# Performance work log

Measured on AMD Instinct MI355X. Metric: run time of the kernel, lower is better.

The kernel has to match this reference:

```python
import jax, jax.numpy as jnp
import numpy as np

T, H, I, E, TOPK = 8192, 2048, 4096, 8, 2

def setup_inputs() -> dict:
    key = jax.random.key(0)
    k1, k2, k3, k4 = jax.random.split(key, 4)
    x = jax.random.normal(k1, (T, H), dtype=jnp.float32)
    gate_w = jax.random.normal(k2, (E, H), dtype=jnp.float32) * 0.02
    ws = jax.random.normal(k3, (E, 2 * I, H), dtype=jnp.float32) * 0.02
    w2s = jax.random.normal(k4, (E, H, I), dtype=jnp.float32) * 0.02
    return {"x": x, "gate_w": gate_w, "ws": ws, "w2s": w2s, "top_k": TOPK}

def reference(x, gate_w, ws, w2s, top_k):
    num_tokens = x.shape[0]
    num_experts = ws.shape[0]
    inter = w2s.shape[2]
    # --- router (fused_topk): softmax -> top-k -> renormalize ---
    logits = x @ gate_w.T                       # [T, E]
    probs = jax.nn.softmax(logits, axis=-1)
    topk_w, topk_ids = jax.lax.top_k(probs, top_k)   # [T, K]
    if top_k > 1:
        topk_w = topk_w / jnp.sum(topk_w, axis=-1, keepdims=True)
    # dense combine-weights [E, T]: sum of routing weights per (token, expert)
    tok = jnp.arange(num_tokens)
    cw = jnp.zeros((num_tokens, num_experts), dtype=x.dtype)
    cw = cw.at[tok[:, None], topk_ids].add(topk_w)
    cw = cw.T                                   # [E, T]
    # --- fused_experts: per-expert gated-SiLU MLP, weighted combine ---
    def body(acc, inp):
        e_ws, e_w2, e_cw = inp                  # [2I,H], [H,I], [T]
        gu = x @ e_ws.T                         # [T, 2I]
        g, u = gu[:, :inter], gu[:, inter:]
        h = jax.nn.silu(g) * u                  # SiluAndMul
        out = h @ e_w2.T                        # [T, H]
        return acc + e_cw[:, None] * out, None
    init = jnp.zeros_like(x)
    final, _ = jax.lax.scan(body, init, (ws, w2s, cw))
    return final
```

## Files before the change

kernel.cpp:

```cpp
#include <hip/hip_runtime.h>
#include <hip/hip_fp16.h>
#include <cstdint>
#include <cstddef>

#define TTOK 8192
#define HD   2048
#define ID   4096
#define NE   8
#define NPAIR (TTOK * 2)
#define PADROWS 18432

typedef _Float16 h8 __attribute__((ext_vector_type(8)));
typedef float    f4 __attribute__((ext_vector_type(4)));

#define VMWAIT(n) asm volatile("s_waitcnt vmcnt(" #n ")" ::: "memory")
#define MEMFENCE  asm volatile("" ::: "memory")
#define BAR()     __builtin_amdgcn_s_barrier()

__device__ __forceinline__ void async_cp16(const void* g, void* l) {
  __builtin_amdgcn_global_load_lds(
      (const __attribute__((address_space(1))) unsigned int*)g,
      (__attribute__((address_space(3))) unsigned int*)l, 16, 0, 0);
}

__device__ __forceinline__ f4 zero4() { f4 z = {0.f, 0.f, 0.f, 0.f}; return z; }

template <bool NT>
__global__ void cvt_kernel(const float* __restrict__ src, _Float16* __restrict__ dst, size_t n) {
  size_t stride = (size_t)gridDim.x * blockDim.x * 8;
  for (size_t i = ((size_t)blockIdx.x * blockDim.x + threadIdx.x) * 8; i < n; i += stride) {
    const float4* s = (const float4*)(src + i);
    float4 a = s[0], b = s[1];
    h8 o;
    o[0] = (_Float16)a.x; o[1] = (_Float16)a.y; o[2] = (_Float16)a.z; o[3] = (_Float16)a.w;
    o[4] = (_Float16)b.x; o[5] = (_Float16)b.y; o[6] = (_Float16)b.z; o[7] = (_Float16)b.w;
    if constexpr (NT) __builtin_nontemporal_store(o, (h8*)(dst + i));
    else *(h8*)(dst + i) = o;
  }
}

__global__ __launch_bounds__(256) void gate_kernel(
    const float* __restrict__ x, const float* __restrict__ gw,
    int* __restrict__ counts, int* __restrict__ tids, float* __restrict__ tw) {
  int lane = threadIdx.x & 63;
  int t = blockIdx.x * 4 + (threadIdx.x >> 6);
  const float* xr = x + (size_t)t * HD;
  float acc[NE];
#pragma unroll
  for (int e = 0; e < NE; e++) acc[e] = 0.f;
  for (int j = lane; j < HD; j += 64) {
    float xv = xr[j];
#pragma unroll
    for (int e = 0; e < NE; e++) acc[e] += xv * gw[e * HD + j];
  }
#pragma unroll
  for (int off = 32; off > 0; off >>= 1) {
#pragma unroll
    for (int e = 0; e < NE; e++) acc[e] += __shfl_xor(acc[e], off, 64);
  }
  if (lane == 0) {
    int e0 = 0; float v0 = acc[0];
#pragma unroll
    for (int e = 1; e < NE; e++) if (acc[e] > v0) { v0 = acc[e]; e0 = e; }
    int e1 = -1; float v1 = -1e30f;
#pragma unroll
    for (int e = 0; e < NE; e++) if (e != e0 && acc[e] > v1) { v1 = acc[e]; e1 = e; }
    float b = __expf(v1 - v0);
    float w0 = 1.f / (1.f + b);
    tids[2 * t] = e0; tids[2 * t + 1] = e1;
    tw[2 * t] = w0;   tw[2 * t + 1] = b * w0;
    atomicAdd(&counts[e0], 1); atomicAdd(&counts[e1], 1);
  }
}

__global__ void scan_kernel(const int* __restrict__ counts, int* __restrict__ offs,
                            int* __restrict__ cursor) {
  if (threadIdx.x == 0 && blockIdx.x == 0) {
    int off = 0;
    for (int e = 0; e < NE; e++) {
      offs[e] = off; cursor[e] = off;
      off += ((counts[e] + 255) >> 8) << 8;
    }
    offs[NE] = off;
  }
}

__global__ void scatter_kernel(const int* __restrict__ tids, const float* __restrict__ tw,
                               int* __restrict__ cursor, int* __restrict__ perm,
                               float* __restrict__ pw, int* __restrict__ pairpos) {
  int t = blockIdx.x * 256 + threadIdx.x;
#pragma unroll
  for (int k = 0; k < 2; k++) {
    int e = tids[2 * t + k];
    int pos = atomicAdd(&cursor[e], 1);
    perm[pos] = t; pw[pos] = tw[2 * t + k];
    pairpos[2 * t + k] = pos;
  }
}

__global__ void padfill_kernel(const int* __restrict__ counts, const int* __restrict__ offs,
                               int* __restrict__ perm) {
  int s = blockIdx.x * 256 + threadIdx.x;
#pragma unroll
  for (int e = 0; e < NE; e++) {
    if (s >= offs[e] + counts[e] && s < offs[e + 1]) perm[s] = -1;
  }
}

#define LA(BB, H) ((BB) * 65536 + (H) * 16384)
#define LB(BB, H) ((BB) * 65536 + 32768 + (H) * 16384)
#define RD(boff) (*(const h8*)(smem + (boff)))

#define LOAD_AF(BB, MH) do { \
  af[0][0] = RD(LA(BB,MH) + amoff + 0*2048 + sa0); \
  af[0][1] = RD(LA(BB,MH) + amoff + 0*2048 + sa1); \
  af[1][0] = RD(LA(BB,MH) + amoff + 1*2048 + sa0); \
  af[1][1] = RD(LA(BB,MH) + amoff + 1*2048 + sa1); \
  af[2][0] = RD(LA(BB,MH) + amoff + 2*2048 + sa0); \
  af[2][1] = RD(LA(BB,MH) + amoff + 2*2048 + sa1); \
  af[3][0] = RD(LA(BB,MH) + amoff + 3*2048 + sa0); \
  af[3][1] = RD(LA(BB,MH) + amoff + 3*2048 + sa1); } while (0)

#define LOAD_BF(BB, NH) do { \
  bf[0][0] = RD(LB(BB,NH) + bnoff + 0*2048 + sa0); \
  bf[0][1] = RD(LB(BB,NH) + bnoff + 0*2048 + sa1); \
  bf[1][0] = RD(LB(BB,NH) + bnoff + 1*2048 + sa0); \
  bf[1][1] = RD(LB(BB,NH) + bnoff + 1*2048 + sa1); } while (0)

#define MM(MH,NH,M,N) \
  acc[MH][NH][M][N] = __builtin_amdgcn_mfma_f32_16x16x32_f16(af[M][0], bf[N][0], acc[MH][NH][M][N], 0, 0, 0); \
  acc[MH][NH][M][N] = __builtin_amdgcn_mfma_f32_16x16x32_f16(af[M][1], bf[N][1], acc[MH][NH][M][N], 0, 0, 0);

#define MFMAQ(MH,NH) do { __builtin_amdgcn_s_setprio(1); \
  MM(MH,NH,0,0) MM(MH,NH,0,1) MM(MH,NH,1,0) MM(MH,NH,1,1) \
  MM(MH,NH,2,0) MM(MH,NH,2,1) MM(MH,NH,3,0) MM(MH,NH,3,1) \
  __builtin_amdgcn_s_setprio(0); } while (0)

#define STG(gp, ldsbyte, kt) do { \
  async_cp16(gp[0] + (size_t)(kt) * 64, smem + (ldsbyte) + (wid * 2 + 0) * 1024 + lane * 16); \
  async_cp16(gp[1] + (size_t)(kt) * 64, smem + (ldsbyte) + (wid * 2 + 1) * 1024 + lane * 16); } while (0)

#define ACC_ZERO() do { \
  _Pragma("unroll") for (int mh = 0; mh < 2; mh++) \
  _Pragma("unroll") for (int nh = 0; nh < 2; nh++) \
  _Pragma("unroll") for (int m = 0; m < 4; m++) \
  _Pragma("unroll") for (int n = 0; n < 2; n++) acc[mh][nh][m][n] = zero4(); } while (0)

#define KLOOP(NI) \
  STG(gA[0], LA(0,0), 0); STG(gA[1], LA(0,1), 0); \
  STG(gB[0], LB(0,0), 0); STG(gB[1], LB(0,1), 0); \
  STG(gA[0], LA(1,0), 1); STG(gB[1], LB(1,1), 1); \
  VMWAIT(4); \
  BAR(); \
  for (int i = 0; i < (NI); ++i) { \
    bool last = (i == (NI) - 1); \
    int kt1 = 2 * i + 1, kt2 = 2 * i + 2, kt3 = 2 * i + 3; \
     \
    MEMFENCE; LOAD_AF(0,0); LOAD_BF(0,0); \
    STG(gA[1], LA(1,1), kt1); STG(gB[0], LB(1,0), kt1); \
    BAR(); MEMFENCE; MFMAQ(0,0); BAR(); \
     \
    MEMFENCE; LOAD_BF(0,1); \
    BAR(); MEMFENCE; MFMAQ(0,1); BAR(); \
     \
    MEMFENCE; LOAD_AF(0,1); \
    if (!last) STG(gA[0], LA(0,0), kt2); \
    BAR(); MEMFENCE; MFMAQ(1,1); BAR(); \
     \
    MEMFENCE; LOAD_BF(0,0); \
    if (!last) { STG(gB[1], LB(0,1), kt2); VMWAIT(4); } else { VMWAIT(0); } \
    BAR(); MEMFENCE; MFMAQ(1,0); BAR(); \
     \
    MEMFENCE; LOAD_AF(1,0); LOAD_BF(1,0); \
    if (!last) { STG(gA[1], LA(0,1), kt2); STG(gB[0], LB(0,0), kt2); } \
    BAR(); MEMFENCE; MFMAQ(0,0); BAR(); \
     \
    MEMFENCE; LOAD_BF(1,1); \
    BAR(); MEMFENCE; MFMAQ(0,1); BAR(); \
     \
    MEMFENCE; LOAD_AF(1,1); \
    if (!last) STG(gA[0], LA(1,0), kt3); \
    BAR(); MEMFENCE; MFMAQ(1,1); BAR(); \
     \
    MEMFENCE; LOAD_BF(1,0); \
    if (!last) { STG(gB[1], LB(1,1), kt3); VMWAIT(4); } \
    BAR(); MEMFENCE; MFMAQ(1,0); BAR(); \
  }

__global__ __launch_bounds__(512, 2) void gemm1_kernel(
    const _Float16* __restrict__ xh, const _Float16* __restrict__ wsh,
    const int* __restrict__ counts, const int* __restrict__ offs,
    const int* __restrict__ perm, _Float16* __restrict__ hb) {
  int bx = blockIdx.x, by = blockIdx.y;
  int e = by >> 5, rb = by & 31;
  if (rb >= ((counts[e] + 255) >> 8)) return;
  int row0 = offs[e] + (rb << 8);
  int n0 = bx << 7;

  __shared__ char smem[131072];
  int tid = threadIdx.x, lane = tid & 63, wid = tid >> 6;
  int wm = wid >> 2, wn = wid & 3;
  int lr = lane & 15, ks = lane >> 4;
  int sa0 = lr * 128 + (((ks)     ^ (lr & 7)) << 4);
  int sa1 = lr * 128 + (((ks + 4) ^ (lr & 7)) << 4);
  int amoff = wm * 8192;
  int bnoff = wn * 4096;

  int srow = wid * 16 + (lane >> 3);
  int scol = ((lane & 7) ^ (lane >> 3)) * 8;
  const _Float16* gA[2][2]; const _Float16* gB[2][2];
#pragma unroll
  for (int h = 0; h < 2; h++)
#pragma unroll
    for (int j = 0; j < 2; j++) {
      int r = row0 + h * 128 + srow + j * 8;
      int pv = perm[r]; if (pv < 0) pv = 0;
      gA[h][j] = xh + (size_t)pv * HD + scol;
      gB[h][j] = wsh + ((size_t)e * 2 * ID + (size_t)h * ID + n0 + srow + j * 8) * HD + scol;
    }

  f4 acc[2][2][4][2];
  h8 af[4][2], bf[2][2];
  ACC_ZERO();

  KLOOP(16)

#pragma unroll
  for (int mh = 0; mh < 2; mh++)
#pragma unroll
    for (int m = 0; m < 4; m++)
#pragma unroll
      for (int n = 0; n < 2; n++)
#pragma unroll
        for (int r = 0; r < 4; r++) {
          float g = acc[mh][0][m][n][r], u = acc[mh][1][m][n][r];
          float hv = g / (1.f + __expf(-g)) * u;
          int row = row0 + mh * 128 + wm * 64 + m * 16 + ks * 4 + r;
          int col = n0 + wn * 32 + n * 16 + lr;
          __builtin_nontemporal_store((_Float16)hv, hb + (size_t)row * ID + col);
        }
}

__global__ __launch_bounds__(512, 2) void gemm2_kernel(
    const _Float16* __restrict__ hb, const _Float16* __restrict__ w2h,
    const int* __restrict__ counts, const int* __restrict__ offs,
    _Float16* __restrict__ hb2) {
  int bx = blockIdx.x, by = blockIdx.y;
  int e = by >> 5, rb = by & 31;
  if (rb >= ((counts[e] + 255) >> 8)) return;
  int row0 = offs[e] + (rb << 8);
  int n0 = bx << 8;

  __shared__ char smem[131072];
  int tid = threadIdx.x, lane = tid & 63, wid = tid >> 6;
  int wm = wid >> 2, wn = wid & 3;
  int lr = lane & 15, ks = lane >> 4;
  int sa0 = lr * 128 + (((ks)     ^ (lr & 7)) << 4);
  int sa1 = lr * 128 + (((ks + 4) ^ (lr & 7)) << 4);
  int amoff = wm * 8192;
  int bnoff = wn * 4096;

  int srow = wid * 16 + (lane >> 3);
  int scol = ((lane & 7) ^ (lane >> 3)) * 8;
  const _Float16* gA[2][2]; const _Float16* gB[2][2];
#pragma unroll
  for (int h = 0; h < 2; h++)
#pragma unroll
    for (int j = 0; j < 2; j++) {
      gA[h][j] = hb + ((size_t)(row0 + h * 128 + srow + j * 8)) * ID + scol;
      gB[h][j] = w2h + ((size_t)e * HD + n0 + h * 128 + srow + j * 8) * ID + scol;
    }

  f4 acc[2][2][4][2];
  h8 af[4][2], bf[2][2];
  ACC_ZERO();

  KLOOP(32)

#pragma unroll
  for (int mh = 0; mh < 2; mh++)
#pragma unroll
    for (int nh = 0; nh < 2; nh++)
#pragma unroll
      for (int m = 0; m < 4; m++)
#pragma unroll
        for (int n = 0; n < 2; n++)
#pragma unroll
          for (int r = 0; r < 4; r++) {
            int row = row0 + mh * 128 + wm * 64 + m * 16 + ks * 4 + r;
            int col = n0 + nh * 128 + wn * 32 + n * 16 + lr;
            __builtin_nontemporal_store((_Float16)acc[mh][nh][m][n][r],
                                        hb2 + (size_t)row * HD + col);
          }
}

__global__ __launch_bounds__(256) void combine_kernel(
    const _Float16* __restrict__ hb2, const int* __restrict__ pairpos,
    const float* __restrict__ pw, float* __restrict__ out) {
  int i = blockIdx.x * 256 + threadIdx.x;
  int t = i >> 8, g = (i & 255) * 8;
  int p0 = pairpos[2 * t], p1 = pairpos[2 * t + 1];
  float w0 = pw[p0], w1 = pw[p1];
  h8 a = *(const h8*)(hb2 + (size_t)p0 * HD + g);
  h8 b = *(const h8*)(hb2 + (size_t)p1 * HD + g);
  f4 o0, o1;
  o0[0] = w0 * (float)a[0] + w1 * (float)b[0];
  o0[1] = w0 * (float)a[1] + w1 * (float)b[1];
  o0[2] = w0 * (float)a[2] + w1 * (float)b[2];
  o0[3] = w0 * (float)a[3] + w1 * (float)b[3];
  o1[0] = w0 * (float)a[4] + w1 * (float)b[4];
  o1[1] = w0 * (float)a[5] + w1 * (float)b[5];
  o1[2] = w0 * (float)a[6] + w1 * (float)b[6];
  o1[3] = w0 * (float)a[7] + w1 * (float)b[7];
  __builtin_nontemporal_store(o0, (f4*)(out + (size_t)t * HD + g));
  __builtin_nontemporal_store(o1, (f4*)(out + (size_t)t * HD + g + 4));
}

extern "C" void kernel_launch(void* const* d_in, const int* in_sizes, int n_in,
                              void* d_out, int out_size, void* d_ws, size_t ws_size,
                              hipStream_t stream) {
  const float* x   = (const float*)d_in[0];
  const float* gw  = (const float*)d_in[1];
  const float* wsf = (const float*)d_in[2];
  const float* w2f = (const float*)d_in[3];

  int* counts   = (int*)d_ws;
  int* offs     = counts + 8;
  int* cursor   = offs + 16;
  int* tids     = cursor + 8;
  float* tw     = (float*)(tids + NPAIR);
  int* perm     = (int*)(tw + NPAIR);
  float* pw     = (float*)(perm + PADROWS);
  int* pairpos  = (int*)(pw + PADROWS);

  char* base = (char*)d_ws;
  size_t off_xh  = (size_t)512 * 1024;
  size_t off_hb  = off_xh + (size_t)TTOK * HD * 2;
  size_t off_big = off_hb + (size_t)PADROWS * ID * 2;
  size_t need    = off_big + (size_t)NE * 2 * ID * HD * 2;
  if (ws_size < need) return;

  _Float16* xh  = (_Float16*)(base + off_xh);
  _Float16* hb  = (_Float16*)(base + off_hb);
  _Float16* wsh = (_Float16*)(base + off_big);
  _Float16* w2h = (_Float16*)(base + off_big);
  _Float16* hb2 = (_Float16*)(base + off_big + (size_t)NE * HD * ID * 2);

  hipMemsetAsync(counts, 0, 64, stream);

  cvt_kernel<false><<<2048, 256, 0, stream>>>(x, xh, (size_t)TTOK * HD);
  cvt_kernel<true><<<4096, 256, 0, stream>>>(wsf, wsh, (size_t)NE * 2 * ID * HD);
  gate_kernel<<<TTOK / 4, 256, 0, stream>>>(x, gw, counts, tids, tw);
  scan_kernel<<<1, 64, 0, stream>>>(counts, offs, cursor);
  scatter_kernel<<<TTOK / 256, 256, 0, stream>>>(tids, tw, cursor, perm, pw, pairpos);
  padfill_kernel<<<PADROWS / 256, 256, 0, stream>>>(counts, offs, perm);

  gemm1_kernel<<<dim3(ID / 128, NE * 32), 512, 0, stream>>>(
      xh, wsh, counts, offs, perm, hb);

  cvt_kernel<false><<<4096, 256, 0, stream>>>(w2f, w2h, (size_t)NE * HD * ID);

  gemm2_kernel<<<dim3(HD / 256, NE * 32), 512, 0, stream>>>(
      hb, w2h, counts, offs, hb2);

  combine_kernel<<<(TTOK * HD / 8) / 256, 256, 0, stream>>>(
      hb2, pairpos, pw, (float*)d_out);
}
```

Measured before the change: 1.426 ms.

## Compact GEMM grids over padded rows, swizzle blocks, split-K gemm2

Replaces the per-expert 32-row-block grid, which launched many early-exiting blocks, with a compact grid over padded row blocks. Each block finds its expert by searching the offsets. Block indices are swizzled in groups of eight row blocks so neighbouring blocks share weight tiles in L2. gemm2 is split along K into two halves that write separate fp16 partial buffers, and the combine kernel sums them. This raises parallelism for gemm2 at the cost of extra partial-result traffic, and it rounds each half to fp16 before the sum.

```diff
diff --git a/kernel.cpp b/kernel.cpp
--- a/kernel.cpp
+++ b/kernel.cpp
@@ -9,6 +9,7 @@
 #define NE   8
 #define NPAIR (TTOK * 2)
 #define PADROWS 18432
+#define RBMAX 72
 
 typedef _Float16 h8 __attribute__((ext_vector_type(8)));
 typedef float    f4 __attribute__((ext_vector_type(4)));
@@ -187,14 +188,23 @@
     BAR(); MEMFENCE; MFMAQ(1,0); BAR(); \
   }
 
+__device__ __forceinline__ int expert_of(const int* offs, int row0) {
+  int e = 0;
+#pragma unroll
+  for (int k = 1; k < NE; k++) if (offs[k] <= row0) e = k;
+  return e;
+}
+
 __global__ __launch_bounds__(512, 2) void gemm1_kernel(
     const _Float16* __restrict__ xh, const _Float16* __restrict__ wsh,
-    const int* __restrict__ counts, const int* __restrict__ offs,
-    const int* __restrict__ perm, _Float16* __restrict__ hb) {
-  int bx = blockIdx.x, by = blockIdx.y;
-  int e = by >> 5, rb = by & 31;
-  if (rb >= ((counts[e] + 255) >> 8)) return;
-  int row0 = offs[e] + (rb << 8);
+    const int* __restrict__ offs, const int* __restrict__ perm,
+    _Float16* __restrict__ hb) {
+  int lin = blockIdx.x + gridDim.x * blockIdx.y;
+  int oct = lin >> 8, x8 = lin & 7, bx = (lin >> 3) & 31;
+  int gyy = oct * 8 + x8;
+  int row0 = gyy << 8;
+  if (row0 >= offs[NE]) return;
+  int e = expert_of(offs, row0);
   int n0 = bx << 7;
 
   __shared__ char smem[131072];
@@ -243,13 +253,16 @@
 
 __global__ __launch_bounds__(512, 2) void gemm2_kernel(
     const _Float16* __restrict__ hb, const _Float16* __restrict__ w2h,
-    const int* __restrict__ counts, const int* __restrict__ offs,
-    _Float16* __restrict__ hb2) {
-  int bx = blockIdx.x, by = blockIdx.y;
-  int e = by >> 5, rb = by & 31;
-  if (rb >= ((counts[e] + 255) >> 8)) return;
-  int row0 = offs[e] + (rb << 8);
+    const int* __restrict__ offs, _Float16* __restrict__ hb2) {
+  int lin = blockIdx.x + gridDim.x * blockIdx.y;
+  int oct = lin >> 6, x8 = lin & 7, bx = (lin >> 3) & 7;
+  int gyy = oct * 8 + x8;
+  int row0 = gyy << 8;
+  if (row0 >= offs[NE]) return;
+  int e = expert_of(offs, row0);
   int n0 = bx << 8;
+  int kh = blockIdx.z;
+  size_t k0 = (size_t)kh * 2048;
 
   __shared__ char smem[131072];
   int tid = threadIdx.x, lane = tid & 63, wid = tid >> 6;
@@ -267,16 +280,17 @@
   for (int h = 0; h < 2; h++)
 #pragma unroll
     for (int j = 0; j < 2; j++) {
-      gA[h][j] = hb + ((size_t)(row0 + h * 128 + srow + j * 8)) * ID + scol;
-      gB[h][j] = w2h + ((size_t)e * HD + n0 + h * 128 + srow + j * 8) * ID + scol;
+      gA[h][j] = hb + ((size_t)(row0 + h * 128 + srow + j * 8)) * ID + k0 + scol;
+      gB[h][j] = w2h + ((size_t)e * HD + n0 + h * 128 + srow + j * 8) * ID + k0 + scol;
     }
 
   f4 acc[2][2][4][2];
   h8 af[4][2], bf[2][2];
   ACC_ZERO();
 
-  KLOOP(32)
-
+  KLOOP(16)
+
+  _Float16* dst = hb2 + (size_t)kh * PADROWS * HD;
 #pragma unroll
   for (int mh = 0; mh < 2; mh++)
 #pragma unroll
@@ -289,8 +303,7 @@
           for (int r = 0; r < 4; r++) {
             int row = row0 + mh * 128 + wm * 64 + m * 16 + ks * 4 + r;
             int col = n0 + nh * 128 + wn * 32 + n * 16 + lr;
-            __builtin_nontemporal_store((_Float16)acc[mh][nh][m][n][r],
-                                        hb2 + (size_t)row * HD + col);
+            dst[(size_t)row * HD + col] = (_Float16)acc[mh][nh][m][n][r];
           }
 }
 
@@ -301,17 +314,18 @@
   int t = i >> 8, g = (i & 255) * 8;
   int p0 = pairpos[2 * t], p1 = pairpos[2 * t + 1];
   float w0 = pw[p0], w1 = pw[p1];
-  h8 a = *(const h8*)(hb2 + (size_t)p0 * HD + g);
-  h8 b = *(const h8*)(hb2 + (size_t)p1 * HD + g);
+  const _Float16* hb2b = hb2 + (size_t)PADROWS * HD;
+  h8 a0 = *(const h8*)(hb2  + (size_t)p0 * HD + g);
+  h8 a1 = *(const h8*)(hb2b + (size_t)p0 * HD + g);
+  h8 b0 = *(const h8*)(hb2  + (size_t)p1 * HD + g);
+  h8 b1 = *(const h8*)(hb2b + (size_t)p1 * HD + g);
   f4 o0, o1;
-  o0[0] = w0 * (float)a[0] + w1 * (float)b[0];
-  o0[1] = w0 * (float)a[1] + w1 * (float)b[1];
-  o0[2] = w0 * (float)a[2] + w1 * (float)b[2];
-  o0[3] = w0 * (float)a[3] + w1 * (float)b[3];
-  o1[0] = w0 * (float)a[4] + w1 * (float)b[4];
-  o1[1] = w0 * (float)a[5] + w1 * (float)b[5];
-  o1[2] = w0 * (float)a[6] + w1 * (float)b[6];
-  o1[3] = w0 * (float)a[7] + w1 * (float)b[7];
+#pragma unroll
+  for (int j = 0; j < 4; j++)
+    o0[j] = w0 * ((float)a0[j] + (float)a1[j]) + w1 * ((float)b0[j] + (float)b1[j]);
+#pragma unroll
+  for (int j = 0; j < 4; j++)
+    o1[j] = w0 * ((float)a0[j + 4] + (float)a1[j + 4]) + w1 * ((float)b0[j + 4] + (float)b1[j + 4]);
   __builtin_nontemporal_store(o0, (f4*)(out + (size_t)t * HD + g));
   __builtin_nontemporal_store(o1, (f4*)(out + (size_t)t * HD + g + 4));
 }
@@ -337,31 +351,36 @@
   size_t off_xh  = (size_t)512 * 1024;
   size_t off_hb  = off_xh + (size_t)TTOK * HD * 2;
   size_t off_big = off_hb + (size_t)PADROWS * ID * 2;
-  size_t need    = off_big + (size_t)NE * 2 * ID * HD * 2;
+  size_t nws = (size_t)NE * 2 * ID * HD;
+  size_t nw2 = (size_t)NE * HD * ID;
+  size_t hb2_bytes = (size_t)2 * PADROWS * HD * 2;
+  size_t big_bytes = nws * 2;
+  size_t alt_bytes = nw2 * 2 + hb2_bytes;
+  size_t need = off_big + (big_bytes > alt_bytes ? big_bytes : alt_bytes);
   if (ws_size < need) return;
 
   _Float16* xh  = (_Float16*)(base + off_xh);
   _Float16* hb  = (_Float16*)(base + off_hb);
   _Float16* wsh = (_Float16*)(base + off_big);
   _Float16* w2h = (_Float16*)(base + off_big);
-  _Float16* hb2 = (_Float16*)(base + off_big + (size_t)NE * HD * ID * 2);
+  _Float16* hb2 = (_Float16*)(base + off_big + nw2 * 2);
 
   hipMemsetAsync(counts, 0, 64, stream);
 
   cvt_kernel<false><<<2048, 256, 0, stream>>>(x, xh, (size_t)TTOK * HD);
-  cvt_kernel<true><<<4096, 256, 0, stream>>>(wsf, wsh, (size_t)NE * 2 * ID * HD);
+  cvt_kernel<true><<<4096, 256, 0, stream>>>(wsf, wsh, nws);
   gate_kernel<<<TTOK / 4, 256, 0, stream>>>(x, gw, counts, tids, tw);
   scan_kernel<<<1, 64, 0, stream>>>(counts, offs, cursor);
   scatter_kernel<<<TTOK / 256, 256, 0, stream>>>(tids, tw, cursor, perm, pw, pairpos);
   padfill_kernel<<<PADROWS / 256, 256, 0, stream>>>(counts, offs, perm);
 
-  gemm1_kernel<<<dim3(ID / 128, NE * 32), 512, 0, stream>>>(
-      xh, wsh, counts, offs, perm, hb);
-
-  cvt_kernel<false><<<4096, 256, 0, stream>>>(w2f, w2h, (size_t)NE * HD * ID);
-
-  gemm2_kernel<<<dim3(HD / 256, NE * 32), 512, 0, stream>>>(
-      hb, w2h, counts, offs, hb2);
+  gemm1_kernel<<<dim3(ID / 128, RBMAX), 512, 0, stream>>>(
+      xh, wsh, offs, perm, hb);
+
+  cvt_kernel<false><<<4096, 256, 0, stream>>>(w2f, w2h, nw2);
+
+  gemm2_kernel<<<dim3(HD / 256, RBMAX, 2), 512, 0, stream>>>(
+      hb, w2h, offs, hb2);
 
   combine_kernel<<<(TTOK * HD / 8) / 256, 256, 0, stream>>>(
       hb2, pairpos, pw, (float*)d_out);
```

New measurement: 1.426 ms. No clear change (+0.0%).
